# Kernel tuning notes

Hardware: AMD Instinct MI355X
Metric: run time of the kernel (lower is better)

Reference implementation:

```python
import jax, jax.numpy as jnp
import numpy as np
from jax import lax

OVERLAP_THRESHOLD = 0.5


def _pairwise_iou(a, b):
    # a: [A,4], b: [B,4] -> [A,B]  (jaccard() in the original repo)
    max_xy = jnp.minimum(a[:, None, 2:], b[None, :, 2:])
    min_xy = jnp.maximum(a[:, None, :2], b[None, :, :2])
    wh = jnp.clip(max_xy - min_xy, 0.0)
    inter = wh[..., 0] * wh[..., 1]
    area_a = (a[:, 2] - a[:, 0]) * (a[:, 3] - a[:, 1])
    area_b = (b[:, 2] - b[:, 0]) * (b[:, 3] - b[:, 1])
    union = area_a[:, None] + area_b[None, :] - inter
    return inter / union


def _elementwise_iou(a, b):
    # matches UBR_ZERO_IoULoss._intersect/_iou_loss: same-shape [K,4] boxes
    max_xy = jnp.minimum(a[:, 2:], b[:, 2:])
    min_xy = jnp.maximum(a[:, :2], b[:, :2])
    wh = jnp.clip(max_xy - min_xy, 0.0)
    inter = wh[:, 0] * wh[:, 1]
    area_a = (a[:, 2] - a[:, 0]) * (a[:, 3] - a[:, 1])
    area_b = (b[:, 2] - b[:, 0]) * (b[:, 3] - b[:, 1])
    return inter / (area_a + area_b - inter)


def _inverse_transform(boxes, deltas):
    w = boxes[:, 2] - boxes[:, 0] + 1.0
    h = boxes[:, 3] - boxes[:, 1] + 1.0
    cx = boxes[:, 0] + 0.5 * w
    cy = boxes[:, 1] + 0.5 * h
    pcx = deltas[:, 0] * w + cx
    pcy = deltas[:, 1] * h + cy
    pw = jnp.exp(deltas[:, 2]) * w
    ph = jnp.exp(deltas[:, 3]) * h
    return jnp.stack([pcx - 0.5 * pw, pcy - 0.5 * ph,
                      pcx + 0.5 * pw, pcy + 0.5 * ph], axis=1)


def setup_inputs() -> dict:
    key = jax.random.key(0)
    k1, k2, k3, k4 = jax.random.split(key, 4)
    N, M, D = 32768, 4096, 512
    raw = jax.random.uniform(k1, (N, 4), dtype=jnp.float32)
    xy = raw[:, :2] * 900.0
    wh = raw[:, 2:] * 100.0 + 1.0
    rois = jnp.concatenate([xy, xy + wh], axis=1)
    # gt boxes = jittered subset of rois -> guarantees IoU>0.5 matches exist
    gt_box = rois[:M] + jax.random.normal(k2, (M, 4), dtype=jnp.float32) * 2.0
    bbox_pred = jax.random.normal(k3, (N, 4), dtype=jnp.float32) * 0.1
    feat = jax.random.normal(k4, (N, D), dtype=jnp.float32)
    return {"rois": rois, "bbox_pred": bbox_pred, "gt_box": gt_box, "feat": feat}


def reference(rois, bbox_pred, gt_box, feat):
    num_rois = rois.shape[0]
    iou = _pairwise_iou(rois, gt_box)              # [N, M]
    max_iou = jnp.max(iou, axis=1)                 # [N]
    max_gt_idx = jnp.argmax(iou, axis=1)           # [N]
    # boolean compaction in torch replaced by a fixed-shape mask (jit-safe)
    mask = lax.stop_gradient((max_iou > OVERLAP_THRESHOLD).astype(rois.dtype))
    n_matched = jnp.sum(mask).astype(jnp.int32)
    matched_gt = gt_box[max_gt_idx]                # [N, 4]
    refined = _inverse_transform(rois, bbox_pred)  # [N, 4]
    iou_ref = _elementwise_iou(refined, matched_gt)
    loss = -jnp.log(iou_ref + 0.1) * mask          # per-roi, 0 where unmatched
    feat_loss = jnp.sum(jnp.abs(jnp.sum(feat * mask[:, None], axis=0)))
    return loss, n_matched, num_rois, refined * mask[:, None], feat_loss
```

## Files before the change

kernel.cpp:

```cpp
#include <hip/hip_runtime.h>
#include <math.h>

#define K3B 512
#define K3R 64
#define GRID 16
#define NCELL 256
#define MAXC 1024

typedef unsigned long long ull;

__device__ __forceinline__ int cell_of(float cx, float cy) {
  int ix = (int)floorf((cx + 16.0f) * 0.015625f);
  int iy = (int)floorf((cy + 16.0f) * 0.015625f);
  ix = min(max(ix, 0), GRID - 1);
  iy = min(max(iy, 0), GRID - 1);
  return iy * GRID + ix;
}

__global__ __launch_bounds__(256) void k_count(
    const float4* __restrict__ rois4, const float4* __restrict__ gt4,
    int* __restrict__ cnt_r, int* __restrict__ cnt_g, int N, int M) {
  int i = blockIdx.x * blockDim.x + threadIdx.x;
  if (i < N) {
    float4 r = rois4[i];
    atomicAdd(&cnt_r[cell_of(0.5f * (r.x + r.z), 0.5f * (r.y + r.w))], 1);
  }
  if (i < M) {
    float4 g = gt4[i];
    atomicAdd(&cnt_g[cell_of(0.5f * (g.x + g.z), 0.5f * (g.y + g.w))], 1);
  }
}

__global__ __launch_bounds__(256) void k_prefix(
    const int* __restrict__ cnt_g, const int* __restrict__ cnt_r,
    int* __restrict__ off_g, int* __restrict__ off_r) {
  __shared__ int s[NCELL];
  int t = threadIdx.x;
  int v = cnt_g[t];
  s[t] = v; __syncthreads();
  for (int o = 1; o < NCELL; o <<= 1) {
    int a = (t >= o) ? s[t - o] : 0; __syncthreads();
    s[t] += a; __syncthreads();
  }
  off_g[t] = s[t] - v;
  __syncthreads();
  v = cnt_r[t];
  s[t] = v; __syncthreads();
  for (int o = 1; o < NCELL; o <<= 1) {
    int a = (t >= o) ? s[t - o] : 0; __syncthreads();
    s[t] += a; __syncthreads();
  }
  off_r[t] = s[t] - v;
}

__global__ __launch_bounds__(256) void k_scatter(
    const float4* __restrict__ rois4, const float4* __restrict__ gt4,
    const int* __restrict__ off_r, const int* __restrict__ off_g,
    int* __restrict__ fill_r, int* __restrict__ fill_g,
    int* __restrict__ ridx, int* __restrict__ gidx, int N, int M) {
  int i = blockIdx.x * blockDim.x + threadIdx.x;
  if (i < N) {
    float4 r = rois4[i];
    int c = cell_of(0.5f * (r.x + r.z), 0.5f * (r.y + r.w));
    ridx[off_r[c] + atomicAdd(&fill_r[c], 1)] = i;
  }
  if (i < M) {
    float4 g = gt4[i];
    int c = cell_of(0.5f * (g.x + g.z), 0.5f * (g.y + g.w));
    gidx[off_g[c] + atomicAdd(&fill_g[c], 1)] = i;
  }
}

__global__ __launch_bounds__(256) void k_main(
    const float4* __restrict__ rois4, const float4* __restrict__ deltas4,
    const float4* __restrict__ gt4,
    const int* __restrict__ off_g, const int* __restrict__ cnt_g,
    const int* __restrict__ gidx,
    const int* __restrict__ off_r, const int* __restrict__ cnt_r,
    const int* __restrict__ ridx,
    float* __restrict__ mask, float* __restrict__ out_loss,
    float* __restrict__ out_refined) {
  const int cellid = blockIdx.x;
  const int cx = cellid & (GRID - 1), cy = cellid >> 4;
  __shared__ float4 sbox[MAXC];
  __shared__ float  sarea[MAXC];
  const int t = threadIdx.x;

  int nc = 0;
  for (int dy = -1; dy <= 1; ++dy) {
    int yy = cy + dy;
    if (yy < 0 || yy > GRID - 1) continue;
    int c0 = (yy << 4) | max(cx - 1, 0);
    int c1 = (yy << 4) | min(cx + 1, GRID - 1);
    int s = off_g[c0];
    int e = off_g[c1] + cnt_g[c1];
    int len = e - s;
    if (nc + len > MAXC) len = MAXC - nc;
    for (int k = t; k < len; k += 256) {
      float4 g = gt4[gidx[s + k]];
      sbox[nc + k] = g;
      sarea[nc + k] = (g.z - g.x) * (g.w - g.y);
    }
    nc += len;
  }
  __syncthreads();

  const double Cd = 0.500000029802322387695312500;
  const int rs = off_r[cellid], rn = cnt_r[cellid];
  for (int base = 0; base < rn; base += 256) {
    int u = base + t;
    if (u >= rn) break;
    int i = ridx[rs + u];
    float4 r = rois4[i];
    float area_a = (r.z - r.x) * (r.w - r.y);

    float bi = 0.f, bu = 1.f;
    int bj = 0;
    bool matched = false;
    for (int j = 0; j < nc; ++j) {
      float4 g = sbox[j];
      float ab = sarea[j];
      float ix = fminf(r.z, g.z) - fmaxf(r.x, g.x);
      float iy = fminf(r.w, g.w) - fmaxf(r.y, g.y);
      float inter = fmaxf(ix, 0.f) * fmaxf(iy, 0.f);
      float uni = (area_a + ab) - inter;
      bool upos = uni > 0.f;
      float ug = upos ? uni : 3.0e38f;
      matched = matched | (fma(-Cd, (double)ug, (double)inter) > 0.0);
      bool win = upos && (inter * bu > bi * uni);
      bi = win ? inter : bi;
      bu = win ? uni : bu;
      bj = win ? j : bj;
    }
    float m = matched ? 1.f : 0.f;
    mask[i] = m;

    float4 d = deltas4[i];
    float w = r.z - r.x + 1.f, h = r.w - r.y + 1.f;
    float ccx = r.x + 0.5f * w, ccy = r.y + 0.5f * h;
    float pcx = d.x * w + ccx, pcy = d.y * h + ccy;
    float pw = expf(d.z) * w, ph = expf(d.w) * h;
    float rx0 = pcx - 0.5f * pw, ry0 = pcy - 0.5f * ph;
    float rx1 = pcx + 0.5f * pw, ry1 = pcy + 0.5f * ph;

    float loss = 0.f;
    if (matched) {
      float4 g = sbox[bj];
      float ix = fmaxf(fminf(rx1, g.z) - fmaxf(rx0, g.x), 0.f);
      float iy = fmaxf(fminf(ry1, g.w) - fmaxf(ry0, g.y), 0.f);
      float inter = ix * iy;
      float aa = (rx1 - rx0) * (ry1 - ry0);
      float ab = (g.z - g.x) * (g.w - g.y);
      float er = inter / (aa + ab - inter);
      loss = -logf(er + 0.1f);
    }
    out_loss[i] = loss;
    out_refined[4 * i + 0] = rx0 * m;
    out_refined[4 * i + 1] = ry0 * m;
    out_refined[4 * i + 2] = rx1 * m;
    out_refined[4 * i + 3] = ry1 * m;
  }
}

__global__ __launch_bounds__(256) void k_feat(
    const float4* __restrict__ feat4, const float* __restrict__ mask,
    float4* __restrict__ pcols4, int D4) {
  const int n0 = blockIdx.x * K3R;
  const int t = threadIdx.x;
  float mv = mask[n0 + (t & 63)];
  ull bits = __ballot(mv != 0.f);

  const int c = t & 127;
  const int p = t >> 7;
  float4 acc = {0.f, 0.f, 0.f, 0.f};
  for (int rr = p; rr < K3R; rr += 16) {
    float4 v[8];
    float sc[8];
    #pragma unroll
    for (int k = 0; k < 8; ++k) {
      int row = rr + 2 * k;
      v[k] = feat4[(size_t)(n0 + row) * D4 + c];
      sc[k] = (float)((bits >> row) & 1ull);
    }
    #pragma unroll
    for (int k = 0; k < 8; ++k) {
      acc.x = fmaf(v[k].x, sc[k], acc.x);
      acc.y = fmaf(v[k].y, sc[k], acc.y);
      acc.z = fmaf(v[k].z, sc[k], acc.z);
      acc.w = fmaf(v[k].w, sc[k], acc.w);
    }
  }
  __shared__ float4 red[256];
  red[t] = acc;
  __syncthreads();
  if (t < 128) {
    float4 o = red[t + 128];
    acc = red[t];
    acc.x += o.x; acc.y += o.y; acc.z += o.z; acc.w += o.w;
    pcols4[(size_t)blockIdx.x * D4 + t] = acc;
  }
}

__global__ __launch_bounds__(256) void k_red1(
    const float4* __restrict__ pcols4, float4* __restrict__ pcols2, int D4) {
  const int c = threadIdx.x & 127;
  const int h = threadIdx.x >> 7;
  const int per = K3B / 64;
  float4 acc = {0.f, 0.f, 0.f, 0.f};
  for (int r = 0; r < per / 2; ++r) {
    float4 v = pcols4[(size_t)(blockIdx.x * per + h * (per / 2) + r) * D4 + c];
    acc.x += v.x; acc.y += v.y; acc.z += v.z; acc.w += v.w;
  }
  __shared__ float4 red[256];
  red[threadIdx.x] = acc;
  __syncthreads();
  if (threadIdx.x < 128) {
    float4 o = red[threadIdx.x + 128];
    acc = red[threadIdx.x];
    acc.x += o.x; acc.y += o.y; acc.z += o.z; acc.w += o.w;
    pcols2[(size_t)blockIdx.x * D4 + threadIdx.x] = acc;
  }
}

__global__ __launch_bounds__(512) void k_final(
    const float* __restrict__ pcols2, const float* __restrict__ mask,
    float* __restrict__ out, int N, int D) {
  const int t = threadIdx.x;
  float s = 0.f;
  for (int r = 0; r < 64; ++r) s += pcols2[(size_t)r * D + t];
  float a = fabsf(s);
  float cnt = 0.f;
  for (int n = t; n < N; n += 512) cnt += mask[n];

  for (int off = 32; off > 0; off >>= 1) {
    a += __shfl_down(a, off, 64);
    cnt += __shfl_down(cnt, off, 64);
  }
  __shared__ float ra[8], rc[8];
  int w = t >> 6;
  if ((t & 63) == 0) { ra[w] = a; rc[w] = cnt; }
  __syncthreads();
  if (t == 0) {
    float ta = 0.f, tc = 0.f;
    for (int k = 0; k < 8; ++k) { ta += ra[k]; tc += rc[k]; }
    out[N] = tc;
    out[N + 1] = (float)N;
    out[(size_t)5 * N + 2] = ta;
  }
}

extern "C" void kernel_launch(void* const* d_in, const int* in_sizes, int n_in,
                              void* d_out, int out_size, void* d_ws, size_t ws_size,
                              hipStream_t stream) {
  const float* rois = (const float*)d_in[0];
  const float* bbox = (const float*)d_in[1];
  const float* gt   = (const float*)d_in[2];
  const float* feat = (const float*)d_in[3];
  const int N = in_sizes[0] / 4;
  const int M = in_sizes[2] / 4;
  const int D = in_sizes[3] / N;
  float* out = (float*)d_out;

  char* ws = (char*)d_ws;
  int* cnt_g = (int*)ws;
  int* cnt_r = cnt_g + NCELL;
  int* fill_g = cnt_r + NCELL;
  int* fill_r = fill_g + NCELL;
  int* off_g = fill_r + NCELL;
  int* off_r = off_g + NCELL;
  int* gidx = off_r + NCELL;
  int* ridx = gidx + M;
  float* mask = (float*)(ridx + N);
  float* pcols = mask + N;
  float* pcols2 = pcols + (size_t)K3B * D;

  hipMemsetAsync(cnt_g, 0, 4 * NCELL * sizeof(int), stream);

  k_count<<<N / 256, 256, 0, stream>>>((const float4*)rois, (const float4*)gt,
                                       cnt_r, cnt_g, N, M);
  k_prefix<<<1, 256, 0, stream>>>(cnt_g, cnt_r, off_g, off_r);
  k_scatter<<<N / 256, 256, 0, stream>>>((const float4*)rois, (const float4*)gt,
                                         off_r, off_g, fill_r, fill_g, ridx, gidx, N, M);
  k_main<<<NCELL, 256, 0, stream>>>((const float4*)rois, (const float4*)bbox,
                                    (const float4*)gt, off_g, cnt_g, gidx,
                                    off_r, cnt_r, ridx, mask, out, out + N + 2);
  k_feat<<<K3B, 256, 0, stream>>>((const float4*)feat, mask, (float4*)pcols, D / 4);
  k_red1<<<64, 256, 0, stream>>>((const float4*)pcols, (float4*)pcols2, D / 4);
  k_final<<<1, 512, 0, stream>>>(pcols2, mask, out, N, D);
}
```

Before: 186.6 us.

## Compact matched rois into a list and sum only their feature rows

The main kernel now appends matched roi indices to a compacted list through an atomic counter instead of writing a dense mask. The feature-sum kernel reads only those matched rows and accumulates column sums with float atomics, which removes the full dense read of feat and the two-stage partial reduction. GT binning and prefix sums move into a single-block kernel that also zeroes the accumulators, cutting launches and a memset. The atomic float accumulation makes the summation order nondeterministic, and the single-block GT binning serializes that work.

```diff
diff --git a/kernel.cpp b/kernel.cpp
--- a/kernel.cpp
+++ b/kernel.cpp
@@ -1,8 +1,6 @@
 #include <hip/hip_runtime.h>
 #include <math.h>
 
-#define K3B 512
-#define K3R 64
 #define GRID 16
 #define NCELL 256
 #define MAXC 1024
@@ -17,57 +15,64 @@
   return iy * GRID + ix;
 }
 
-__global__ __launch_bounds__(256) void k_count(
-    const float4* __restrict__ rois4, const float4* __restrict__ gt4,
-    int* __restrict__ cnt_r, int* __restrict__ cnt_g, int N, int M) {
+__global__ __launch_bounds__(256) void k_count_r(
+    const float4* __restrict__ rois4, int* __restrict__ cnt_r, int N) {
   int i = blockIdx.x * blockDim.x + threadIdx.x;
   if (i < N) {
     float4 r = rois4[i];
     atomicAdd(&cnt_r[cell_of(0.5f * (r.x + r.z), 0.5f * (r.y + r.w))], 1);
   }
-  if (i < M) {
-    float4 g = gt4[i];
-    atomicAdd(&cnt_g[cell_of(0.5f * (g.x + g.z), 0.5f * (g.y + g.w))], 1);
-  }
-}
-
-__global__ __launch_bounds__(256) void k_prefix(
-    const int* __restrict__ cnt_g, const int* __restrict__ cnt_r,
-    int* __restrict__ off_g, int* __restrict__ off_r) {
-  __shared__ int s[NCELL];
-  int t = threadIdx.x;
-  int v = cnt_g[t];
-  s[t] = v; __syncthreads();
+}
+
+__global__ __launch_bounds__(256) void k_bin(
+    const float4* __restrict__ gt4, int M,
+    int* __restrict__ off_g, int* __restrict__ cnt_g, int* __restrict__ gidx,
+    const int* __restrict__ cnt_r, int* __restrict__ off_r, int* __restrict__ fill_r,
+    float* __restrict__ pcols, int* __restrict__ ctr) {
+  __shared__ int scnt[NCELL], spre[NCELL], sfill[NCELL];
+  const int t = threadIdx.x;
+  scnt[t] = 0;
+  __syncthreads();
+  for (int k = t; k < M; k += 256) {
+    float4 g = gt4[k];
+    atomicAdd(&scnt[cell_of(0.5f * (g.x + g.z), 0.5f * (g.y + g.w))], 1);
+  }
+  __syncthreads();
+  int v = scnt[t];
+  spre[t] = v; __syncthreads();
   for (int o = 1; o < NCELL; o <<= 1) {
-    int a = (t >= o) ? s[t - o] : 0; __syncthreads();
-    s[t] += a; __syncthreads();
-  }
-  off_g[t] = s[t] - v;
-  __syncthreads();
-  v = cnt_r[t];
-  s[t] = v; __syncthreads();
+    int a = (t >= o) ? spre[t - o] : 0; __syncthreads();
+    spre[t] += a; __syncthreads();
+  }
+  int ex = spre[t] - v;
+  off_g[t] = ex; cnt_g[t] = v; sfill[t] = ex;
+  __syncthreads();
+  for (int k = t; k < M; k += 256) {
+    float4 g = gt4[k];
+    int c = cell_of(0.5f * (g.x + g.z), 0.5f * (g.y + g.w));
+    gidx[atomicAdd(&sfill[c], 1)] = k;
+  }
+  int vr = cnt_r[t];
+  __syncthreads();
+  spre[t] = vr; __syncthreads();
   for (int o = 1; o < NCELL; o <<= 1) {
-    int a = (t >= o) ? s[t - o] : 0; __syncthreads();
-    s[t] += a; __syncthreads();
-  }
-  off_r[t] = s[t] - v;
-}
-
-__global__ __launch_bounds__(256) void k_scatter(
-    const float4* __restrict__ rois4, const float4* __restrict__ gt4,
-    const int* __restrict__ off_r, const int* __restrict__ off_g,
-    int* __restrict__ fill_r, int* __restrict__ fill_g,
-    int* __restrict__ ridx, int* __restrict__ gidx, int N, int M) {
+    int a = (t >= o) ? spre[t - o] : 0; __syncthreads();
+    spre[t] += a; __syncthreads();
+  }
+  int exr = spre[t] - vr;
+  off_r[t] = exr; fill_r[t] = exr;
+  pcols[t] = 0.f; pcols[t + 256] = 0.f;
+  if (t == 0) *ctr = 0;
+}
+
+__global__ __launch_bounds__(256) void k_scatter_r(
+    const float4* __restrict__ rois4, int* __restrict__ fill_r,
+    int* __restrict__ ridx, int N) {
   int i = blockIdx.x * blockDim.x + threadIdx.x;
   if (i < N) {
     float4 r = rois4[i];
     int c = cell_of(0.5f * (r.x + r.z), 0.5f * (r.y + r.w));
-    ridx[off_r[c] + atomicAdd(&fill_r[c], 1)] = i;
-  }
-  if (i < M) {
-    float4 g = gt4[i];
-    int c = cell_of(0.5f * (g.x + g.z), 0.5f * (g.y + g.w));
-    gidx[off_g[c] + atomicAdd(&fill_g[c], 1)] = i;
+    ridx[atomicAdd(&fill_r[c], 1)] = i;
   }
 }
 
@@ -78,8 +83,8 @@
     const int* __restrict__ gidx,
     const int* __restrict__ off_r, const int* __restrict__ cnt_r,
     const int* __restrict__ ridx,
-    float* __restrict__ mask, float* __restrict__ out_loss,
-    float* __restrict__ out_refined) {
+    int* __restrict__ ctr, int* __restrict__ mlist,
+    float* __restrict__ out_loss, float* __restrict__ out_refined) {
   const int cellid = blockIdx.x;
   const int cx = cellid & (GRID - 1), cy = cellid >> 4;
   __shared__ float4 sbox[MAXC];
@@ -93,8 +98,7 @@
     int c0 = (yy << 4) | max(cx - 1, 0);
     int c1 = (yy << 4) | min(cx + 1, GRID - 1);
     int s = off_g[c0];
-    int e = off_g[c1] + cnt_g[c1];
-    int len = e - s;
+    int len = off_g[c1] + cnt_g[c1] - s;
     if (nc + len > MAXC) len = MAXC - nc;
     for (int k = t; k < len; k += 256) {
       float4 g = gt4[gidx[s + k]];
@@ -133,7 +137,7 @@
       bj = win ? j : bj;
     }
     float m = matched ? 1.f : 0.f;
-    mask[i] = m;
+    if (matched) mlist[atomicAdd(ctr, 1)] = i;
 
     float4 d = deltas4[i];
     float w = r.z - r.x + 1.f, h = r.w - r.y + 1.f;
@@ -162,88 +166,45 @@
   }
 }
 
-__global__ __launch_bounds__(256) void k_feat(
-    const float4* __restrict__ feat4, const float* __restrict__ mask,
-    float4* __restrict__ pcols4, int D4) {
-  const int n0 = blockIdx.x * K3R;
-  const int t = threadIdx.x;
-  float mv = mask[n0 + (t & 63)];
-  ull bits = __ballot(mv != 0.f);
-
+__global__ __launch_bounds__(256) void k_feat2(
+    const float4* __restrict__ feat4, const int* __restrict__ mlist,
+    const int* __restrict__ ctr, float* __restrict__ pcols, int D4) {
+  const int nm = *ctr;
+  const int t = threadIdx.x;
   const int c = t & 127;
-  const int p = t >> 7;
+  const int h = t >> 7;
   float4 acc = {0.f, 0.f, 0.f, 0.f};
-  for (int rr = p; rr < K3R; rr += 16) {
-    float4 v[8];
-    float sc[8];
-    #pragma unroll
-    for (int k = 0; k < 8; ++k) {
-      int row = rr + 2 * k;
-      v[k] = feat4[(size_t)(n0 + row) * D4 + c];
-      sc[k] = (float)((bits >> row) & 1ull);
-    }
-    #pragma unroll
-    for (int k = 0; k < 8; ++k) {
-      acc.x = fmaf(v[k].x, sc[k], acc.x);
-      acc.y = fmaf(v[k].y, sc[k], acc.y);
-      acc.z = fmaf(v[k].z, sc[k], acc.z);
-      acc.w = fmaf(v[k].w, sc[k], acc.w);
-    }
+  for (int e = blockIdx.x * 2 + h; e < nm; e += 2 * gridDim.x) {
+    int row = mlist[e];
+    float4 v = feat4[(size_t)row * D4 + c];
+    acc.x += v.x; acc.y += v.y; acc.z += v.z; acc.w += v.w;
   }
   __shared__ float4 red[256];
   red[t] = acc;
   __syncthreads();
   if (t < 128) {
     float4 o = red[t + 128];
-    acc = red[t];
     acc.x += o.x; acc.y += o.y; acc.z += o.z; acc.w += o.w;
-    pcols4[(size_t)blockIdx.x * D4 + t] = acc;
-  }
-}
-
-__global__ __launch_bounds__(256) void k_red1(
-    const float4* __restrict__ pcols4, float4* __restrict__ pcols2, int D4) {
-  const int c = threadIdx.x & 127;
-  const int h = threadIdx.x >> 7;
-  const int per = K3B / 64;
-  float4 acc = {0.f, 0.f, 0.f, 0.f};
-  for (int r = 0; r < per / 2; ++r) {
-    float4 v = pcols4[(size_t)(blockIdx.x * per + h * (per / 2) + r) * D4 + c];
-    acc.x += v.x; acc.y += v.y; acc.z += v.z; acc.w += v.w;
-  }
-  __shared__ float4 red[256];
-  red[threadIdx.x] = acc;
-  __syncthreads();
-  if (threadIdx.x < 128) {
-    float4 o = red[threadIdx.x + 128];
-    acc = red[threadIdx.x];
-    acc.x += o.x; acc.y += o.y; acc.z += o.z; acc.w += o.w;
-    pcols2[(size_t)blockIdx.x * D4 + threadIdx.x] = acc;
+    atomicAdd(&pcols[4 * t + 0], acc.x);
+    atomicAdd(&pcols[4 * t + 1], acc.y);
+    atomicAdd(&pcols[4 * t + 2], acc.z);
+    atomicAdd(&pcols[4 * t + 3], acc.w);
   }
 }
 
 __global__ __launch_bounds__(512) void k_final(
-    const float* __restrict__ pcols2, const float* __restrict__ mask,
-    float* __restrict__ out, int N, int D) {
-  const int t = threadIdx.x;
-  float s = 0.f;
-  for (int r = 0; r < 64; ++r) s += pcols2[(size_t)r * D + t];
-  float a = fabsf(s);
-  float cnt = 0.f;
-  for (int n = t; n < N; n += 512) cnt += mask[n];
-
-  for (int off = 32; off > 0; off >>= 1) {
-    a += __shfl_down(a, off, 64);
-    cnt += __shfl_down(cnt, off, 64);
-  }
-  __shared__ float ra[8], rc[8];
-  int w = t >> 6;
-  if ((t & 63) == 0) { ra[w] = a; rc[w] = cnt; }
+    const float* __restrict__ pcols, const int* __restrict__ ctr,
+    float* __restrict__ out, int N) {
+  const int t = threadIdx.x;
+  float a = fabsf(pcols[t]);
+  for (int off = 32; off > 0; off >>= 1) a += __shfl_down(a, off, 64);
+  __shared__ float ra[8];
+  if ((t & 63) == 0) ra[t >> 6] = a;
   __syncthreads();
   if (t == 0) {
-    float ta = 0.f, tc = 0.f;
-    for (int k = 0; k < 8; ++k) { ta += ra[k]; tc += rc[k]; }
-    out[N] = tc;
+    float ta = 0.f;
+    for (int k = 0; k < 8; ++k) ta += ra[k];
+    out[N] = (float)(*ctr);
     out[N + 1] = (float)N;
     out[(size_t)5 * N + 2] = ta;
   }
@@ -262,29 +223,27 @@
   float* out = (float*)d_out;
 
   char* ws = (char*)d_ws;
-  int* cnt_g = (int*)ws;
-  int* cnt_r = cnt_g + NCELL;
-  int* fill_g = cnt_r + NCELL;
-  int* fill_r = fill_g + NCELL;
-  int* off_g = fill_r + NCELL;
-  int* off_r = off_g + NCELL;
-  int* gidx = off_r + NCELL;
-  int* ridx = gidx + M;
-  float* mask = (float*)(ridx + N);
-  float* pcols = mask + N;
-  float* pcols2 = pcols + (size_t)K3B * D;
-
-  hipMemsetAsync(cnt_g, 0, 4 * NCELL * sizeof(int), stream);
-
-  k_count<<<N / 256, 256, 0, stream>>>((const float4*)rois, (const float4*)gt,
-                                       cnt_r, cnt_g, N, M);
-  k_prefix<<<1, 256, 0, stream>>>(cnt_g, cnt_r, off_g, off_r);
-  k_scatter<<<N / 256, 256, 0, stream>>>((const float4*)rois, (const float4*)gt,
-                                         off_r, off_g, fill_r, fill_g, ridx, gidx, N, M);
+  int* cnt_r  = (int*)ws;
+  int* off_r  = cnt_r + NCELL;
+  int* fill_r = off_r + NCELL;
+  int* cnt_g  = fill_r + NCELL;
+  int* off_g  = cnt_g + NCELL;
+  int* gidx   = off_g + NCELL;
+  int* ridx   = gidx + M;
+  int* mlist  = ridx + N;
+  int* ctr    = mlist + N;
+  float* pcols = (float*)(ctr + 1);
+
+  hipMemsetAsync(cnt_r, 0, NCELL * sizeof(int), stream);
+
+  k_count_r<<<N / 256, 256, 0, stream>>>((const float4*)rois, cnt_r, N);
+  k_bin<<<1, 256, 0, stream>>>((const float4*)gt, M, off_g, cnt_g, gidx,
+                               cnt_r, off_r, fill_r, pcols, ctr);
+  k_scatter_r<<<N / 256, 256, 0, stream>>>((const float4*)rois, fill_r, ridx, N);
   k_main<<<NCELL, 256, 0, stream>>>((const float4*)rois, (const float4*)bbox,
                                     (const float4*)gt, off_g, cnt_g, gidx,
-                                    off_r, cnt_r, ridx, mask, out, out + N + 2);
-  k_feat<<<K3B, 256, 0, stream>>>((const float4*)feat, mask, (float4*)pcols, D / 4);
-  k_red1<<<64, 256, 0, stream>>>((const float4*)pcols, (float4*)pcols2, D / 4);
-  k_final<<<1, 512, 0, stream>>>(pcols2, mask, out, N, D);
-}
+                                    off_r, cnt_r, ridx, ctr, mlist,
+                                    out, out + N + 2);
+  k_feat2<<<512, 256, 0, stream>>>((const float4*)feat, mlist, ctr, pcols, D / 4);
+  k_final<<<1, 512, 0, stream>>>(pcols, ctr, out, N);
+}
```

New measurement: 232.2 us. 24.4% more time.
